# Optimization experiments

Hardware: AMD Instinct MI355X
Metric: run time of the kernel (lower is better)

Reference implementation:

```python
import jax, jax.numpy as jnp
import numpy as np

EMBED = 768
HEAD = 64
SEQ = 4096
BATCH = 4


def setup_inputs() -> dict:
    key = jax.random.key(0)
    ks = jax.random.split(key, 7)
    s = 1.0 / np.sqrt(EMBED)
    x = jax.random.normal(ks[0], (BATCH, SEQ, EMBED), dtype=jnp.float32)
    Wq = jax.random.uniform(ks[1], (EMBED, HEAD), jnp.float32, -s, s)
    bq = jax.random.uniform(ks[2], (HEAD,), jnp.float32, -s, s)
    Wk = jax.random.uniform(ks[3], (EMBED, HEAD), jnp.float32, -s, s)
    bk = jax.random.uniform(ks[4], (HEAD,), jnp.float32, -s, s)
    Wv = jax.random.uniform(ks[5], (EMBED, HEAD), jnp.float32, -s, s)
    bv = jax.random.uniform(ks[6], (HEAD,), jnp.float32, -s, s)
    return {"x": x, "Wq": Wq, "bq": bq, "Wk": Wk, "bk": bk, "Wv": Wv, "bv": bv}


def reference(x, Wq, bq, Wk, bk, Wv, bv):
    # x: [B,T,E]
    Q = x @ Wq + bq  # [B,T,H]
    K = x @ Wk + bk
    V = x @ Wv + bv
    scale = 1.0 / jnp.sqrt(jnp.asarray(HEAD, dtype=x.dtype))
    wei = jnp.einsum('bqh,bkh->bqk', Q, K) * scale  # [B,T,T]
    T = x.shape[1]
    causal = jnp.tril(jnp.ones((T, T), dtype=bool))
    wei = jnp.where(causal, wei, -jnp.inf)
    wei = jax.nn.softmax(wei, axis=-1)
    return jnp.einsum('bqk,bkh->bqh', wei, V)  # [B,T,H]
```

## Files before the change

kernel.cpp:

```cpp
#include <hip/hip_runtime.h>


#define BB 4
#define TT 4096
#define EE 768
#define HH 64
#define BT (BB*TT)

typedef __attribute__((ext_vector_type(8))) short short8;
typedef __attribute__((ext_vector_type(4))) float f32x4;
#define MFMA16(a,b,c) __builtin_amdgcn_mfma_f32_16x16x32_bf16(a,b,c,0,0,0)
#define QSCALE 0.18033688011112042f

static __device__ __forceinline__ float bflo(unsigned a){ return __uint_as_float(a << 16); }
static __device__ __forceinline__ unsigned short f2bf(float f){
    unsigned x = __float_as_uint(f);
    x += 0x7fffu + ((x >> 16) & 1u);
    return (unsigned short)(x >> 16);
}
template<int FP32>
static __device__ __forceinline__ float ldin(const void* p, int idx){
    if (FP32) return ((const float*)p)[idx];
    return bflo(((const unsigned short*)p)[idx]);
}

template<int FP32>
static __device__ void wt_body(const void* W, int wi, int e0, unsigned short* wt){
    __shared__ unsigned short ts[64 * 72];
    const int tid = threadIdx.x;
    #pragma unroll
    for (int p = 0; p < 2; p++){
        int i = p * 256 + tid;
        int r = i >> 3, g = i & 7;
        unsigned short v[8];
        if (FP32){
            const float* src = (const float*)W + (size_t)(e0 + r) * HH + g * 8;
            const float4 a = *(const float4*)src, b = *(const float4*)(src + 4);
            v[0]=f2bf(a.x); v[1]=f2bf(a.y); v[2]=f2bf(a.z); v[3]=f2bf(a.w);
            v[4]=f2bf(b.x); v[5]=f2bf(b.y); v[6]=f2bf(b.z); v[7]=f2bf(b.w);
        } else {
            const unsigned short* src = (const unsigned short*)W + (size_t)(e0 + r) * HH + g * 8;
            #pragma unroll
            for (int j = 0; j < 8; j++) v[j] = src[j];
        }
        #pragma unroll
        for (int j = 0; j < 8; j++) ts[r * 72 + g * 8 + j] = v[j];
    }
    __syncthreads();
    #pragma unroll
    for (int p = 0; p < 2; p++){
        int i = p * 256 + tid;
        int h = i >> 3, g = i & 7;
        unsigned short v[8];
        #pragma unroll
        for (int j = 0; j < 8; j++) v[j] = ts[(g * 8 + j) * 72 + h];
        unsigned short* dst = wt + (size_t)(wi * 64 + h) * EE + e0 + g * 8;
        uint4 pk;
        pk.x = (unsigned)v[0] | ((unsigned)v[1] << 16);
        pk.y = (unsigned)v[2] | ((unsigned)v[3] << 16);
        pk.z = (unsigned)v[4] | ((unsigned)v[5] << 16);
        pk.w = (unsigned)v[6] | ((unsigned)v[7] << 16);
        *(uint4*)dst = pk;
    }
}
__global__ __launch_bounds__(256) void wt_kernel(
    const unsigned short* xu, const void* Wq, const void* Wk, const void* Wv,
    unsigned short* wt, int* flag){
    __shared__ int cnt;
    const int tid = threadIdx.x;
    if (tid == 0) cnt = 0;
    __syncthreads();
    int c = 0;
    #pragma unroll
    for (int i = 0; i < 16; i++){
        unsigned u = xu[tid * 16 + i];
        unsigned e = (u >> 7) & 0xFFu;
        if (e >= 140u) c++;
    }
    atomicAdd(&cnt, c);
    __syncthreads();
    const int fp32 = (cnt > 32) ? 1 : 0;
    if (blockIdx.x == 0 && tid == 0) *flag = fp32;
    const int wi = blockIdx.x / 12;
    const int e0 = (blockIdx.x % 12) * 64;
    const void* W = (wi == 0) ? Wq : (wi == 1) ? Wk : Wv;
    if (fp32) wt_body<1>(W, wi, e0, wt);
    else      wt_body<0>(W, wi, e0, wt);
}

template<int FP32>
static __device__ void qkv_body(const void* x, const unsigned short* wt,
    const void* bq, const void* bk, const void* bv,
    unsigned short* Qw, unsigned short* Kw, unsigned short* VTw,
    unsigned short* xs, unsigned short* wsl)
{
    const int tid = threadIdx.x, lane = tid & 63, w = tid >> 6;
    const int l15 = lane & 15, quad = lane >> 4;
    const int z = blockIdx.x;
    const int m0 = (z >> 1) * 32;
    const int nh = z & 1;
    const int rh = (w & 1) * 16;
    const int ngl = (w >> 1) * 3;

    f32x4 acc[3];
    #pragma unroll
    for (int i = 0; i < 3; i++) acc[i] = (f32x4)(0.f);

    const int srow = tid >> 3, sg = tid & 7;

    const float*          xsF = (const float*)x + (size_t)(m0 + srow) * EE + sg * 8;
    const unsigned short* xsB = (const unsigned short*)x + (size_t)(m0 + srow) * EE + sg * 8;
    const unsigned short* ws0 = wt + (size_t)(nh * 96 + srow) * EE + sg * 8;
    const unsigned short* ws1 = ws0 + (size_t)32 * EE;
    const unsigned short* ws2 = ws0 + (size_t)64 * EE;

    float4 xa, xb;
    short8 xv;
    short8 wr0, wr1, wr2;

    if (FP32){ xa = *(const float4*)xsF; xb = *(const float4*)(xsF + 4); }
    else     { xv = *(const short8*)xsB; }
    wr0 = *(const short8*)ws0;
    wr1 = *(const short8*)ws1;
    wr2 = *(const short8*)ws2;

    for (int c = 0; c < 12; c++){
        __syncthreads();
        {
            short8 v;
            if (FP32){
                v[0]=(short)f2bf(xa.x); v[1]=(short)f2bf(xa.y); v[2]=(short)f2bf(xa.z); v[3]=(short)f2bf(xa.w);
                v[4]=(short)f2bf(xb.x); v[5]=(short)f2bf(xb.y); v[6]=(short)f2bf(xb.z); v[7]=(short)f2bf(xb.w);
            } else {
                v = xv;
            }
            *(short8*)&xs[srow * 72 + sg * 8] = v;
        }
        *(short8*)&wsl[(     srow) * 72 + sg * 8] = wr0;
        *(short8*)&wsl[(32 + srow) * 72 + sg * 8] = wr1;
        *(short8*)&wsl[(64 + srow) * 72 + sg * 8] = wr2;
        if (c < 11){
            const int c1 = (c + 1) * 64;
            if (FP32){ xa = *(const float4*)(xsF + c1); xb = *(const float4*)(xsF + c1 + 4); }
            else     { xv = *(const short8*)(xsB + c1); }
            wr0 = *(const short8*)(ws0 + c1);
            wr1 = *(const short8*)(ws1 + c1);
            wr2 = *(const short8*)(ws2 + c1);
        }
        __syncthreads();
        #pragma unroll
        for (int kst = 0; kst < 2; kst++){
            const short8 a = *(const short8*)&xs[(rh + l15) * 72 + kst * 32 + quad * 8];
            #pragma unroll
            for (int nf = 0; nf < 3; nf++){
                const short8 bfr = *(const short8*)&wsl[((ngl + nf) * 16 + l15) * 72 + kst * 32 + quad * 8];
                acc[nf] = MFMA16(a, bfr, acc[nf]);
            }
        }
    }
    #pragma unroll
    for (int nf = 0; nf < 3; nf++){
        const int gi = nh * 6 + ngl + nf;
        const int wi = gi >> 2;
        const int h = (gi & 3) * 16 + l15;
        const void* bp = (wi == 0) ? bq : (wi == 1) ? bk : bv;
        const float bias = ldin<FP32>(bp, h);
        if (wi == 0){
            #pragma unroll
            for (int rr = 0; rr < 4; rr++){
                const int tok = m0 + rh + quad * 4 + rr;
                Qw[(size_t)tok * HH + h] = f2bf((acc[nf][rr] + bias) * QSCALE);
            }
        } else if (wi == 1){
            #pragma unroll
            for (int rr = 0; rr < 4; rr++){
                const int tok = m0 + rh + quad * 4 + rr;
                Kw[(size_t)tok * HH + h] = f2bf(acc[nf][rr] + bias);
            }
        } else {
            const int tok0 = m0 + rh + quad * 4;
            const int bloc = tok0 >> 12;
            const int tl = tok0 & 4095;
            uint2 pk;
            pk.x = (unsigned)f2bf(acc[nf][0] + bias) | ((unsigned)f2bf(acc[nf][1] + bias) << 16);
            pk.y = (unsigned)f2bf(acc[nf][2] + bias) | ((unsigned)f2bf(acc[nf][3] + bias) << 16);
            *(uint2*)&VTw[(size_t)(bloc * 64 + h) * TT + tl] = pk;
        }
    }
}
__global__ __launch_bounds__(256, 2) void qkv_kernel(
    const void* x, const unsigned short* wt,
    const void* bq, const void* bk, const void* bv,
    unsigned short* Qw, unsigned short* Kw, unsigned short* VTw, const int* flag){
    __shared__ unsigned short xs[32 * 72];
    __shared__ unsigned short wsl[96 * 72];
    if (*flag) qkv_body<1>(x, wt, bq, bk, bv, Qw, Kw, VTw, xs, wsl);
    else       qkv_body<0>(x, wt, bq, bk, bv, Qw, Kw, VTw, xs, wsl);
}

static __device__ __forceinline__ void qk8(
    const short8 (&qf)[2][2], const short8 (&kf)[4][2], f32x4 (&s)[2][4])
{
    #pragma unroll
    for (int mt = 0; mt < 2; mt++)
        #pragma unroll
        for (int c = 0; c < 4; c++){
            s[mt][c] = (f32x4)(0.f);
            s[mt][c] = MFMA16(qf[mt][0], kf[c][0], s[mt][c]);
            s[mt][c] = MFMA16(qf[mt][1], kf[c][1], s[mt][c]);
        }
}
__global__ __launch_bounds__(512, 2) void attn_kernel(
    const unsigned short* __restrict__ Q,
    const unsigned short* __restrict__ K, const unsigned short* __restrict__ VT,
    void* __restrict__ out, const int* __restrict__ flag)
{
    __shared__ unsigned short sbuf[8][2304];
    __shared__ float lpart[8][32];

    const int mode = *flag;
    const int z = blockIdx.x;
    const int b = z & 3;
    const int qt = 127 - (z >> 2);
    const int q0 = qt * 32;
    const int nkb = (qt >> 1) + 1;
    const int tid = threadIdx.x;
    const int lane = tid & 63;
    const int w = tid >> 6;
    const int l15 = lane & 15, quad = lane >> 4;
    const int brow = b * TT;

    const short8 VONES = (short8)(short)0x3F80;

    f32x4 O[2][4];
    f32x4 Lk[2];
    #pragma unroll
    for (int mt = 0; mt < 2; mt++){
        Lk[mt] = (f32x4)(0.f);
        #pragma unroll
        for (int i = 0; i < 4; i++) O[mt][i] = (f32x4)(0.f);
    }

    if (w < nkb){
        short8 qf[2][2];
        #pragma unroll
        for (int mt = 0; mt < 2; mt++)
            #pragma unroll
            for (int kst = 0; kst < 2; kst++)
                qf[mt][kst] = *(const short8*)(Q + (size_t)(brow + q0 + mt * 16 + l15) * HH + kst * 32 + quad * 8);

        short8 kf[4][2];
        #pragma unroll
        for (int c = 0; c < 4; c++)
            #pragma unroll
            for (int kst = 0; kst < 2; kst++)
                kf[c][kst] = *(const short8*)(K + (size_t)(brow + w * 64 + c * 16 + l15) * HH + kst * 32 + quad * 8);

        f32x4 sacc[2][4];
        qk8(qf, kf, sacc);
        if (w + 8 < nkb){
            const int kn0 = (w + 8) * 64;
            #pragma unroll
            for (int c = 0; c < 4; c++)
                #pragma unroll
                for (int kst = 0; kst < 2; kst++)
                    kf[c][kst] = *(const short8*)(K + (size_t)(brow + kn0 + c * 16 + l15) * HH + kst * 32 + quad * 8);
        }

        for (int u = w; u < nkb; u += 8){
            const int k0 = u * 64;
            short8 vf[4][2];
            #pragma unroll
            for (int c = 0; c < 4; c++)
                #pragma unroll
                for (int kst = 0; kst < 2; kst++)
                    vf[c][kst] = *(const short8*)(VT + (size_t)(b * 64 + c * 16 + l15) * TT + k0 + kst * 32 + quad * 8);
            const bool diag = (u == nkb - 1);
            #pragma unroll
            for (int mt = 0; mt < 2; mt++){
                #pragma unroll
                for (int c = 0; c < 4; c++){
                    #pragma unroll
                    for (int rr = 0; rr < 4; rr++){
                        float sv = sacc[mt][c][rr];
                        if (diag){
                            const int kg = k0 + c * 16 + l15;
                            const int qg = q0 + mt * 16 + quad * 4 + rr;
                            sv = (kg <= qg) ? sv : -1e30f;
                        }
                        const float p = exp2f(sv);
                        sbuf[w][mt * 1152 + (quad * 4 + rr) * 72 + c * 16 + l15] =
                            (unsigned short)(__float_as_uint(p) >> 16);
                    }
                }
            }
            if (u + 8 < nkb){
                qk8(qf, kf, sacc);
                if (u + 16 < nkb){
                    const int kn0 = (u + 16) * 64;
                    #pragma unroll
                    for (int c = 0; c < 4; c++)
                        #pragma unroll
                        for (int kst = 0; kst < 2; kst++)
                            kf[c][kst] = *(const short8*)(K + (size_t)(brow + kn0 + c * 16 + l15) * HH + kst * 32 + quad * 8);
                }
            }
            #pragma unroll
            for (int mt = 0; mt < 2; mt++){
                const short8 pf0 = *(const short8*)&sbuf[w][mt * 1152 + l15 * 72 + quad * 8];
                const short8 pf1 = *(const short8*)&sbuf[w][mt * 1152 + l15 * 72 + 32 + quad * 8];
                Lk[mt] = MFMA16(pf0, VONES, Lk[mt]);
                Lk[mt] = MFMA16(pf1, VONES, Lk[mt]);
                #pragma unroll
                for (int c2 = 0; c2 < 4; c2++){
                    O[mt][c2] = MFMA16(pf0, vf[c2][0], O[mt][c2]);
                    O[mt][c2] = MFMA16(pf1, vf[c2][1], O[mt][c2]);
                }
            }
        }
    }
    #pragma unroll
    for (int mt = 0; mt < 2; mt++)
        #pragma unroll
        for (int rr = 0; rr < 4; rr++){
            const int row = mt * 16 + quad * 4 + rr;
            #pragma unroll
            for (int c2 = 0; c2 < 4; c2++)
                sbuf[w][row * 72 + c2 * 16 + l15] = f2bf(O[mt][c2][rr]);
            if (l15 == 0) lpart[w][row] = Lk[mt][rr];
        }
    __syncthreads();
    #pragma unroll
    for (int i = 0; i < 4; i++){
        const int e = i * 512 + tid;
        const int r = e >> 6, h = e & 63;
        float num = 0.f, den = 0.f;
        #pragma unroll
        for (int ww = 0; ww < 8; ww++){
            num += bflo(sbuf[ww][r * 72 + h]);
            den += lpart[ww][r];
        }
        const float ov = num / den;
        const size_t gi = (size_t)(brow + q0 + r) * HH + h;
        if (mode) ((float*)out)[gi] = ov;
        else      ((unsigned short*)out)[gi] = f2bf(ov);
    }
}

extern "C" void kernel_launch(void* const* d_in, const int* in_sizes, int n_in,
                              void* d_out, int out_size, void* d_ws, size_t ws_size,
                              hipStream_t stream) {
    const void* x  = d_in[0];
    const void* Wq = d_in[1];
    const void* bq = d_in[2];
    const void* Wk = d_in[3];
    const void* bk = d_in[4];
    const void* Wv = d_in[5];
    const void* bv = d_in[6];

    unsigned short* Qw  = (unsigned short*)d_ws;
    unsigned short* Kw  = Qw + (size_t)BT * HH;
    unsigned short* VTw = Kw + (size_t)BT * HH;
    unsigned short* wt  = VTw + (size_t)BT * HH;
    int* flag  = (int*)(wt + (size_t)192 * EE);

    wt_kernel<<<36, 256, 0, stream>>>((const unsigned short*)x, Wq, Wk, Wv, wt, flag);
    qkv_kernel<<<1024, 256, 0, stream>>>(x, wt, bq, bk, bv, Qw, Kw, VTw, flag);
    attn_kernel<<<512, 512, 0, stream>>>(Qw, Kw, VTw, d_out, flag);
}
```

Before: 150.6 us.

## Halve per-wave LDS staging buffer by processing P tiles one row-block at a time

The per-wave shared buffer for probability tiles is halved. The two 16-row tiles are now written and consumed one after another, and the mt=0 PV MFMAs are interleaved before the next QK computation. The final cross-wave reduction is split into two passes with extra barriers. This cuts LDS use per block to allow more resident blocks or less LDS pressure, at the cost of extra LDS round-trips, serialisation and two more __syncthreads in the epilogue.

```diff
diff --git a/kernel.cpp b/kernel.cpp
--- a/kernel.cpp
+++ b/kernel.cpp
@@ -215,8 +215,8 @@
     const unsigned short* __restrict__ K, const unsigned short* __restrict__ VT,
     void* __restrict__ out, const int* __restrict__ flag)
 {
-    __shared__ unsigned short sbuf[8][2304];
-    __shared__ float lpart[8][32];
+    __shared__ unsigned short sbuf[8][1152];
+    __shared__ float lpart[8][16];
 
     const int mode = *flag;
     const int z = blockIdx.x;
@@ -277,9 +277,9 @@
                     vf[c][kst] = *(const short8*)(VT + (size_t)(b * 64 + c * 16 + l15) * TT + k0 + kst * 32 + quad * 8);
             const bool diag = (u == nkb - 1);
             #pragma unroll
-            for (int mt = 0; mt < 2; mt++){
-                #pragma unroll
-                for (int c = 0; c < 4; c++){
+            for (int mt = 0; mt < 2; mt++)
+                #pragma unroll
+                for (int c = 0; c < 4; c++)
                     #pragma unroll
                     for (int rr = 0; rr < 4; rr++){
                         float sv = sacc[mt][c][rr];
@@ -288,12 +288,31 @@
                             const int qg = q0 + mt * 16 + quad * 4 + rr;
                             sv = (kg <= qg) ? sv : -1e30f;
                         }
-                        const float p = exp2f(sv);
-                        sbuf[w][mt * 1152 + (quad * 4 + rr) * 72 + c * 16 + l15] =
-                            (unsigned short)(__float_as_uint(p) >> 16);
+                        sacc[mt][c][rr] = exp2f(sv);
                     }
+            #pragma unroll
+            for (int c = 0; c < 4; c++)
+                #pragma unroll
+                for (int rr = 0; rr < 4; rr++)
+                    sbuf[w][(quad * 4 + rr) * 72 + c * 16 + l15] =
+                        (unsigned short)(__float_as_uint(sacc[0][c][rr]) >> 16);
+            {
+                const short8 pf0 = *(const short8*)&sbuf[w][l15 * 72 + quad * 8];
+                const short8 pf1 = *(const short8*)&sbuf[w][l15 * 72 + 32 + quad * 8];
+                Lk[0] = MFMA16(pf0, VONES, Lk[0]);
+                Lk[0] = MFMA16(pf1, VONES, Lk[0]);
+                #pragma unroll
+                for (int c2 = 0; c2 < 4; c2++){
+                    O[0][c2] = MFMA16(pf0, vf[c2][0], O[0][c2]);
+                    O[0][c2] = MFMA16(pf1, vf[c2][1], O[0][c2]);
                 }
             }
+            #pragma unroll
+            for (int c = 0; c < 4; c++)
+                #pragma unroll
+                for (int rr = 0; rr < 4; rr++)
+                    sbuf[w][(quad * 4 + rr) * 72 + c * 16 + l15] =
+                        (unsigned short)(__float_as_uint(sacc[1][c][rr]) >> 16);
             if (u + 8 < nkb){
                 qk8(qf, kf, sacc);
                 if (u + 16 < nkb){
@@ -305,45 +324,46 @@
                             kf[c][kst] = *(const short8*)(K + (size_t)(brow + kn0 + c * 16 + l15) * HH + kst * 32 + quad * 8);
                 }
             }
-            #pragma unroll
-            for (int mt = 0; mt < 2; mt++){
-                const short8 pf0 = *(const short8*)&sbuf[w][mt * 1152 + l15 * 72 + quad * 8];
-                const short8 pf1 = *(const short8*)&sbuf[w][mt * 1152 + l15 * 72 + 32 + quad * 8];
-                Lk[mt] = MFMA16(pf0, VONES, Lk[mt]);
-                Lk[mt] = MFMA16(pf1, VONES, Lk[mt]);
+            {
+                const short8 pf0 = *(const short8*)&sbuf[w][l15 * 72 + quad * 8];
+                const short8 pf1 = *(const short8*)&sbuf[w][l15 * 72 + 32 + quad * 8];
+                Lk[1] = MFMA16(pf0, VONES, Lk[1]);
+                Lk[1] = MFMA16(pf1, VONES, Lk[1]);
                 #pragma unroll
                 for (int c2 = 0; c2 < 4; c2++){
-                    O[mt][c2] = MFMA16(pf0, vf[c2][0], O[mt][c2]);
-                    O[mt][c2] = MFMA16(pf1, vf[c2][1], O[mt][c2]);
+                    O[1][c2] = MFMA16(pf0, vf[c2][0], O[1][c2]);
+                    O[1][c2] = MFMA16(pf1, vf[c2][1], O[1][c2]);
                 }
             }
         }
     }
-    #pragma unroll
-    for (int mt = 0; mt < 2; mt++)
+    #pragma unroll 1
+    for (int mt = 0; mt < 2; mt++){
         #pragma unroll
         for (int rr = 0; rr < 4; rr++){
-            const int row = mt * 16 + quad * 4 + rr;
+            const int row = quad * 4 + rr;
             #pragma unroll
             for (int c2 = 0; c2 < 4; c2++)
                 sbuf[w][row * 72 + c2 * 16 + l15] = f2bf(O[mt][c2][rr]);
             if (l15 == 0) lpart[w][row] = Lk[mt][rr];
         }
-    __syncthreads();
-    #pragma unroll
-    for (int i = 0; i < 4; i++){
-        const int e = i * 512 + tid;
-        const int r = e >> 6, h = e & 63;
-        float num = 0.f, den = 0.f;
-        #pragma unroll
-        for (int ww = 0; ww < 8; ww++){
-            num += bflo(sbuf[ww][r * 72 + h]);
-            den += lpart[ww][r];
-        }
-        const float ov = num / den;
-        const size_t gi = (size_t)(brow + q0 + r) * HH + h;
-        if (mode) ((float*)out)[gi] = ov;
-        else      ((unsigned short*)out)[gi] = f2bf(ov);
+        __syncthreads();
+        #pragma unroll
+        for (int i = 0; i < 2; i++){
+            const int e = i * 512 + tid;
+            const int r = e >> 6, h = e & 63;
+            float num = 0.f, den = 0.f;
+            #pragma unroll
+            for (int ww = 0; ww < 8; ww++){
+                num += bflo(sbuf[ww][r * 72 + h]);
+                den += lpart[ww][r];
+            }
+            const float ov = num / den;
+            const size_t gi = (size_t)(brow + q0 + mt * 16 + r) * HH + h;
+            if (mode) ((float*)out)[gi] = ov;
+            else      ((unsigned short*)out)[gi] = f2bf(ov);
+        }
+        __syncthreads();
     }
 }
 
```

Result: slower. 162.6 us (+7.9%).
